# Kernel optimization log

Measured on AMD Instinct MI355X. Metric: run time of the kernel, lower is better.

## Reference

```python
import jax, jax.numpy as jnp
import numpy as np

N_NODES = 100000
N_EDGES = 400000
IN_F, HID, OUT_F = 128, 1024, 64


def gcn_conv(x, src, dst, ew, W, b, n):
    # PyG GCNConv: add self-loops (weight 1), symmetric normalization,
    # out[dst] += norm * (x @ W)[src], then bias.
    loop = jnp.arange(n)
    s = jnp.concatenate([src, loop])
    d = jnp.concatenate([dst, loop])
    w = jnp.concatenate([ew, jnp.ones((n,), dtype=ew.dtype)])
    deg = jax.ops.segment_sum(w, d, num_segments=n)
    dinv = jnp.where(deg > 0, jax.lax.rsqrt(deg), 0.0)
    norm = dinv[s] * w * dinv[d]                      # [E+N]
    h = x @ W                                         # [N, out]
    out = jax.ops.segment_sum(h[s] * norm[:, None], d, num_segments=n)
    return out + b


def setup_inputs() -> dict:
    key = jax.random.key(0)
    k = jax.random.split(key, 8)
    x = jax.random.normal(k[0], (N_NODES, IN_F), dtype=jnp.float32)
    edge_index = jax.random.randint(k[1], (2, N_EDGES), 0, N_NODES, dtype=jnp.int64)
    edge_weight = jax.random.uniform(k[2], (N_EDGES,), dtype=jnp.float32)
    # Glorot-ish init for params
    W1 = jax.random.normal(k[3], (IN_F, HID), dtype=jnp.float32) * (1.0 / np.sqrt(IN_F))
    b1 = jnp.zeros((HID,), dtype=jnp.float32)
    W2 = jax.random.normal(k[4], (HID, OUT_F), dtype=jnp.float32) * (1.0 / np.sqrt(HID))
    b2 = jnp.zeros((OUT_F,), dtype=jnp.float32)
    return {"x": x, "edge_index": edge_index, "edge_weight": edge_weight,
            "W1": W1, "b1": b1, "W2": W2, "b2": b2}


def reference(x, edge_index, edge_weight, W1, b1, W2, b2):
    src, dst = edge_index[0], edge_index[1]
    h = gcn_conv(x, src, dst, edge_weight, W1, b1, N_NODES)
    h = jax.nn.relu(h)
    # F.dropout with training=False is identity (eval mode)
    out = gcn_conv(h, src, dst, edge_weight, W2, b2, N_NODES)
    return out
```

## Files before the change

kernel.cpp:

```cpp
#include <hip/hip_runtime.h>
#include <hip/hip_bf16.h>

#define N_NODES 100000
#define N_EDGES 400000
#define IN_F    128
#define HID     1024
#define OUT_F   64
#define BUCKET_CAP 24

typedef __attribute__((ext_vector_type(8))) short short8;
typedef __attribute__((ext_vector_type(4))) float floatx4;

__device__ inline unsigned short f2bf(float f) {
    unsigned int u = __float_as_uint(f);
    unsigned int r = u + 0x7FFF + ((u >> 16) & 1);
    return (unsigned short)(r >> 16);
}

__device__ inline float bf2f(unsigned int lo16) {
    return __uint_as_float(lo16 << 16);
}

__device__ __forceinline__ void gload_lds16(const void* g, void* l) {
    __builtin_amdgcn_global_load_lds(
        (const __attribute__((address_space(1))) void*)g,
        (__attribute__((address_space(3))) void*)l, 16, 0, 0);
}


__global__ void init_kernel(float* __restrict__ deg, int* __restrict__ cnt, int n) {
    int i = blockIdx.x * blockDim.x + threadIdx.x;
    if (i < n) { deg[i] = 1.0f; cnt[i] = 0; }
}

__global__ void deg_accum_kernel(const int* __restrict__ dst, const float* __restrict__ w,
                                 float* __restrict__ deg, int E) {
    int e = blockIdx.x * blockDim.x + threadIdx.x;
    if (e < E) atomicAdd(&deg[dst[e]], w[e]);
}

__global__ void rsqrt_inplace_kernel(float* __restrict__ deg, int n) {
    int i = blockIdx.x * blockDim.x + threadIdx.x;
    if (i < n) deg[i] = rsqrtf(deg[i]);
}

__global__ void fill_pairs_kernel(const int* __restrict__ src, const int* __restrict__ dst,
                                  const float* __restrict__ w, const float* __restrict__ dinv,
                                  int* __restrict__ cnt, int2* __restrict__ pairs, int E) {
    int e = blockIdx.x * blockDim.x + threadIdx.x;
    if (e < E) {
        int s = src[e];
        int d = dst[e];
        float nv = dinv[s] * w[e] * dinv[d];
        int slot = atomicAdd(&cnt[d], 1);
        if (slot < BUCKET_CAP)
            pairs[(long)d * BUCKET_CAP + slot] = make_int2(s, __float_as_int(nv));
    }
}


__global__ void convert_xb_kernel(const float* __restrict__ in, unsigned short* __restrict__ out, long n8) {
    long i = (long)blockIdx.x * blockDim.x + threadIdx.x;
    if (i < n8) {
        float4 a = ((const float4*)in)[i * 2];
        float4 b = ((const float4*)in)[i * 2 + 1];
        unsigned int q0 = (unsigned int)f2bf(a.x) | ((unsigned int)f2bf(a.y) << 16);
        unsigned int q1 = (unsigned int)f2bf(a.z) | ((unsigned int)f2bf(a.w) << 16);
        unsigned int q2 = (unsigned int)f2bf(b.x) | ((unsigned int)f2bf(b.y) << 16);
        unsigned int q3 = (unsigned int)f2bf(b.z) | ((unsigned int)f2bf(b.w) << 16);
        ((uint4*)out)[i] = make_uint4(q0, q1, q2, q3);
    }
}


__global__ __launch_bounds__(256) void gather128_kernel(
    const int2* __restrict__ pairs, const int* __restrict__ cnt,
    const float* __restrict__ dinv, const unsigned short* __restrict__ xb,
    unsigned short* __restrict__ xab)
{
    int node = blockIdx.x * 4 + (threadIdx.x >> 6);
    int l = threadIdx.x & 63;
    float di = dinv[node];
    float s = di * di;
    unsigned int uv = ((const unsigned int*)(xb + (long)node * IN_F))[l];
    float2 acc;
    acc.x = bf2f(uv & 0xffffu) * s;
    acc.y = bf2f(uv >> 16) * s;
    int c = cnt[node]; c = c < BUCKET_CAP ? c : BUCKET_CAP;
    const int2* p = pairs + (long)node * BUCKET_CAP;
    int j = 0;
    for (; j + 4 <= c; j += 4) {
        int2 p0 = p[j], p1 = p[j + 1], p2 = p[j + 2], p3 = p[j + 3];
        unsigned int u0 = ((const unsigned int*)(xb + (long)p0.x * IN_F))[l];
        unsigned int u1 = ((const unsigned int*)(xb + (long)p1.x * IN_F))[l];
        unsigned int u2 = ((const unsigned int*)(xb + (long)p2.x * IN_F))[l];
        unsigned int u3 = ((const unsigned int*)(xb + (long)p3.x * IN_F))[l];
        float n0 = __int_as_float(p0.y), n1 = __int_as_float(p1.y);
        float n2 = __int_as_float(p2.y), n3 = __int_as_float(p3.y);
        acc.x += n0 * bf2f(u0 & 0xffffu) + n1 * bf2f(u1 & 0xffffu)
               + n2 * bf2f(u2 & 0xffffu) + n3 * bf2f(u3 & 0xffffu);
        acc.y += n0 * bf2f(u0 >> 16) + n1 * bf2f(u1 >> 16)
               + n2 * bf2f(u2 >> 16) + n3 * bf2f(u3 >> 16);
    }
    for (; j < c; j++) {
        int2 pp = p[j];
        float nv = __int_as_float(pp.y);
        unsigned int u = ((const unsigned int*)(xb + (long)pp.x * IN_F))[l];
        acc.x += nv * bf2f(u & 0xffffu);
        acc.y += nv * bf2f(u >> 16);
    }
    unsigned int pk = (unsigned int)f2bf(acc.x) | ((unsigned int)f2bf(acc.y) << 16);
    ((unsigned int*)(xab + (long)node * IN_F))[l] = pk;
}

__global__ __launch_bounds__(256) void gather64_kernel(
    const int2* __restrict__ pairs, const int* __restrict__ cnt,
    const float* __restrict__ dinv, const unsigned short* __restrict__ tb,
    const float* __restrict__ bias, float* __restrict__ out)
{
    int node = blockIdx.x * 8 + (threadIdx.x >> 5);
    int l = threadIdx.x & 31;
    float di = dinv[node];
    float s = di * di;
    unsigned int tv = ((const unsigned int*)(tb + (long)node * OUT_F))[l];
    float2 bb = ((const float2*)bias)[l];
    float2 acc;
    acc.x = bf2f(tv & 0xffffu) * s + bb.x;
    acc.y = bf2f(tv >> 16) * s + bb.y;
    int c = cnt[node]; c = c < BUCKET_CAP ? c : BUCKET_CAP;
    const int2* p = pairs + (long)node * BUCKET_CAP;
    int j = 0;
    for (; j + 4 <= c; j += 4) {
        int2 p0 = p[j], p1 = p[j + 1], p2 = p[j + 2], p3 = p[j + 3];
        unsigned int u0 = ((const unsigned int*)(tb + (long)p0.x * OUT_F))[l];
        unsigned int u1 = ((const unsigned int*)(tb + (long)p1.x * OUT_F))[l];
        unsigned int u2 = ((const unsigned int*)(tb + (long)p2.x * OUT_F))[l];
        unsigned int u3 = ((const unsigned int*)(tb + (long)p3.x * OUT_F))[l];
        float n0 = __int_as_float(p0.y), n1 = __int_as_float(p1.y);
        float n2 = __int_as_float(p2.y), n3 = __int_as_float(p3.y);
        acc.x += n0 * bf2f(u0 & 0xffffu) + n1 * bf2f(u1 & 0xffffu)
               + n2 * bf2f(u2 & 0xffffu) + n3 * bf2f(u3 & 0xffffu);
        acc.y += n0 * bf2f(u0 >> 16) + n1 * bf2f(u1 >> 16)
               + n2 * bf2f(u2 >> 16) + n3 * bf2f(u3 >> 16);
    }
    for (; j < c; j++) {
        int2 pp = p[j];
        float nv = __int_as_float(pp.y);
        unsigned int u = ((const unsigned int*)(tb + (long)pp.x * OUT_F))[l];
        acc.x += nv * bf2f(u & 0xffffu);
        acc.y += nv * bf2f(u >> 16);
    }
    ((float2*)(out + (long)node * OUT_F))[l] = acc;
}


__global__ void convert_wstream_kernel(const float* __restrict__ W1, const float* __restrict__ W2,
                                       unsigned short* __restrict__ S) {
    int r = blockIdx.x * blockDim.x + threadIdx.x;
    int c = blockIdx.y;
    int f = r >> 9;
    int l = (r >> 3) & 63;
    int j = r & 7;
    float v;
    if (f < 16) {
        int nt = f >> 2, kt = f & 3;
        int hid = c * 64 + nt * 16 + (l & 15);
        int k   = kt * 32 + (l >> 4) * 8 + j;
        v = W1[(long)k * HID + hid];
    } else {
        int f2 = f - 16;
        int kb = f2 >> 2, nt = f2 & 3;
        int kh = c * 64 + kb * 32 + (l >> 4) * 8 + j;
        int oc = nt * 16 + (l & 15);
        v = W2[(long)kh * OUT_F + oc];
    }
    S[(long)c * 12288 + r] = f2bf(v);
}


__global__ __launch_bounds__(512, 4) void fused_mlp_mfma_kernel(
    const unsigned short* __restrict__ Xb, const unsigned short* __restrict__ Wstream,
    const float* __restrict__ b1, unsigned short* __restrict__ Tb, int M)
{
    __shared__ unsigned short Wbuf[12288];
    __shared__ unsigned short Hs[8][2048];

    const int tid = threadIdx.x;
    const int w   = tid >> 6;
    const int l   = tid & 63;
    const int lr  = l & 15;
    const int lq  = l >> 4;
    const int swz = (lr & 7) << 4;
    const long row0 = (long)blockIdx.x * 256 + w * 32;

    short8 bx[2][4];
    #pragma unroll
    for (int rt = 0; rt < 2; rt++) {
        long row = row0 + rt * 16 + lr;
        if (row < M) {
            const unsigned short* p = Xb + row * IN_F + lq * 8;
            #pragma unroll
            for (int kt = 0; kt < 4; kt++)
                bx[rt][kt] = *(const short8*)(p + kt * 32);
        } else {
            #pragma unroll
            for (int kt = 0; kt < 4; kt++)
                #pragma unroll
                for (int j = 0; j < 8; j++) bx[rt][kt][j] = 0;
        }
    }

    {
        const unsigned short* g = Wstream + (long)(w * 3) * 512 + l * 8;
        unsigned short* d = &Wbuf[(w * 3) * 512];
        #pragma unroll
        for (int s = 0; s < 3; s++)
            gload_lds16(g + s * 512, d + s * 512);
    }

    floatx4 tacc[2][4];
    #pragma unroll
    for (int rt = 0; rt < 2; rt++)
        #pragma unroll
        for (int nt = 0; nt < 4; nt++)
            tacc[rt][nt] = (floatx4)0.0f;

    for (int c = 0; c < 16; c++) {
        __syncthreads();

        const unsigned short* Wb = &Wbuf[0];
        char* slab = (char*)&Hs[w][0];

        floatx4 hacc[2][4];
        #pragma unroll
        for (int rt = 0; rt < 2; rt++)
            #pragma unroll
            for (int nt = 0; nt < 4; nt++)
                hacc[rt][nt] = (floatx4)0.0f;

        #pragma unroll
        for (int nt = 0; nt < 4; nt++) {
            short8 w1f[4];
            #pragma unroll
            for (int kt = 0; kt < 4; kt++)
                w1f[kt] = *(const short8*)(Wb + (nt * 4 + kt) * 512 + l * 8);
            #pragma unroll
            for (int kt = 0; kt < 4; kt++) {
                hacc[0][nt] = __builtin_amdgcn_mfma_f32_16x16x32_bf16(w1f[kt], bx[0][kt], hacc[0][nt], 0, 0, 0);
                hacc[1][nt] = __builtin_amdgcn_mfma_f32_16x16x32_bf16(w1f[kt], bx[1][kt], hacc[1][nt], 0, 0, 0);
            }
        }

        #pragma unroll
        for (int nt = 0; nt < 4; nt++) {
            floatx4 bb = *(const floatx4*)(b1 + c * 64 + nt * 16 + lq * 4);
            #pragma unroll
            for (int rt = 0; rt < 2; rt++) {
                float h0 = fmaxf(hacc[rt][nt][0] + bb[0], 0.0f);
                float h1 = fmaxf(hacc[rt][nt][1] + bb[1], 0.0f);
                float h2 = fmaxf(hacc[rt][nt][2] + bb[2], 0.0f);
                float h3 = fmaxf(hacc[rt][nt][3] + bb[3], 0.0f);
                unsigned int p0 = (unsigned int)f2bf(h0) | ((unsigned int)f2bf(h1) << 16);
                unsigned int p1 = (unsigned int)f2bf(h2) | ((unsigned int)f2bf(h3) << 16);
                int off = (rt * 16 + lr) * 128 + (((nt * 32) + lq * 8) ^ swz);
                *(uint2*)(slab + off) = make_uint2(p0, p1);
            }
        }

        short8 hf[2][2];
        #pragma unroll
        for (int rt = 0; rt < 2; rt++)
            #pragma unroll
            for (int kb = 0; kb < 2; kb++) {
                int off = (rt * 16 + lr) * 128 + ((kb * 64 + lq * 16) ^ swz);
                hf[rt][kb] = *(const short8*)(slab + off);
            }

        #pragma unroll
        for (int kb = 0; kb < 2; kb++) {
            #pragma unroll
            for (int nt = 0; nt < 4; nt++) {
                short8 w2f = *(const short8*)(Wb + (16 + kb * 4 + nt) * 512 + l * 8);
                tacc[0][nt] = __builtin_amdgcn_mfma_f32_16x16x32_bf16(w2f, hf[0][kb], tacc[0][nt], 0, 0, 0);
                tacc[1][nt] = __builtin_amdgcn_mfma_f32_16x16x32_bf16(w2f, hf[1][kb], tacc[1][nt], 0, 0, 0);
            }
        }

        if (c < 15) {
            __syncthreads();
            const unsigned short* g = Wstream + (long)(c + 1) * 12288 + (long)(w * 3) * 512 + l * 8;
            unsigned short* d = &Wbuf[(w * 3) * 512];
            #pragma unroll
            for (int s = 0; s < 3; s++)
                gload_lds16(g + s * 512, d + s * 512);
        }
    }

    #pragma unroll
    for (int rt = 0; rt < 2; rt++) {
        long row = row0 + rt * 16 + lr;
        if (row < M) {
            #pragma unroll
            for (int nt = 0; nt < 4; nt++) {
                unsigned int q0 = (unsigned int)f2bf(tacc[rt][nt][0]) | ((unsigned int)f2bf(tacc[rt][nt][1]) << 16);
                unsigned int q1 = (unsigned int)f2bf(tacc[rt][nt][2]) | ((unsigned int)f2bf(tacc[rt][nt][3]) << 16);
                *(uint2*)(Tb + row * OUT_F + nt * 16 + lq * 4) = make_uint2(q0, q1);
            }
        }
    }
}


extern "C" void kernel_launch(void* const* d_in, const int* in_sizes, int n_in,
                              void* d_out, int out_size, void* d_ws, size_t ws_size,
                              hipStream_t stream) {
    const float* x   = (const float*)d_in[0];
    const int*   src = (const int*)d_in[1];
    const int*   dst = ((const int*)d_in[1]) + N_EDGES;
    const float* ew  = (const float*)d_in[2];
    const float* W1  = (const float*)d_in[3];
    const float* b1  = (const float*)d_in[4];
    const float* W2  = (const float*)d_in[5];
    const float* b2  = (const float*)d_in[6];
    float* out = (float*)d_out;

    float* ws     = (float*)d_ws;
    float* dinv   = ws;
    int*   cnt    = (int*)(ws + 100096);
    int2*  pairs  = (int2*)(ws + 200192);
    unsigned short* xb  = (unsigned short*)(ws + 5000192);
    unsigned short* xab = (unsigned short*)(ws + 11400192);
    unsigned short* tb  = (unsigned short*)(ws + 17800192);
    unsigned short* wstream = (unsigned short*)(ws + 21000192);

    const int B = 256;

    init_kernel<<<(N_NODES + B - 1) / B, B, 0, stream>>>(dinv, cnt, N_NODES);
    deg_accum_kernel<<<(N_EDGES + B - 1) / B, B, 0, stream>>>(dst, ew, dinv, N_EDGES);
    convert_xb_kernel<<<(int)(((long)N_NODES * IN_F / 8 + B - 1) / B), B, 0, stream>>>(
        x, xb, (long)N_NODES * IN_F / 8);
    convert_wstream_kernel<<<dim3(48, 16), B, 0, stream>>>(W1, W2, wstream);
    rsqrt_inplace_kernel<<<(N_NODES + B - 1) / B, B, 0, stream>>>(dinv, N_NODES);
    fill_pairs_kernel<<<(N_EDGES + B - 1) / B, B, 0, stream>>>(src, dst, ew, dinv, cnt, pairs, N_EDGES);

    gather128_kernel<<<N_NODES / 4, 256, 0, stream>>>(pairs, cnt, dinv, xb, xab);

    fused_mlp_mfma_kernel<<<(N_NODES + 255) / 256, 512, 0, stream>>>(
        xab, wstream, b1, tb, N_NODES);

    gather64_kernel<<<N_NODES / 8, 256, 0, stream>>>(pairs, cnt, dinv, tb, b2, out);
}
```

Before: 184.6 us.

## Double-buffer weight stream and feed hidden activations to MFMA from registers

The fused MLP kernel now double-buffers the LDS weight chunk so the next chunk's global-to-LDS load is issued before computing the current one, removing one barrier per iteration. It also drops the per-wave LDS scratch for the hidden tile: the W2 stream is re-permuted in the conversion kernel so the first MFMA's output register layout maps directly onto the second MFMA's B operand, which avoids the LDS write/read round trip. In exchange the kernel uses about twice the weight LDS, which may change occupancy, and it relies on a more intricate K-index permutation of W2.

```diff
diff --git a/kernel.cpp b/kernel.cpp
--- a/kernel.cpp
+++ b/kernel.cpp
@@ -169,9 +169,9 @@
         v = W1[(long)k * HID + hid];
     } else {
         int f2 = f - 16;
-        int kb = f2 >> 2, nt = f2 & 3;
-        int kh = c * 64 + kb * 32 + (l >> 4) * 8 + j;
-        int oc = nt * 16 + (l & 15);
+        int kb = f2 >> 2, nt2 = f2 & 3;
+        int kh = c * 64 + kb * 32 + (j >> 2) * 16 + (l >> 4) * 4 + (j & 3);
+        int oc = nt2 * 16 + (l & 15);
         v = W2[(long)kh * OUT_F + oc];
     }
     S[(long)c * 12288 + r] = f2bf(v);
@@ -182,15 +182,13 @@
     const unsigned short* __restrict__ Xb, const unsigned short* __restrict__ Wstream,
     const float* __restrict__ b1, unsigned short* __restrict__ Tb, int M)
 {
-    __shared__ unsigned short Wbuf[12288];
-    __shared__ unsigned short Hs[8][2048];
+    __shared__ unsigned short Wbuf[2][12288];
 
     const int tid = threadIdx.x;
     const int w   = tid >> 6;
     const int l   = tid & 63;
     const int lr  = l & 15;
     const int lq  = l >> 4;
-    const int swz = (lr & 7) << 4;
     const long row0 = (long)blockIdx.x * 256 + w * 32;
 
     short8 bx[2][4];
@@ -212,11 +210,12 @@
 
     {
         const unsigned short* g = Wstream + (long)(w * 3) * 512 + l * 8;
-        unsigned short* d = &Wbuf[(w * 3) * 512];
+        unsigned short* d = &Wbuf[0][(w * 3) * 512];
         #pragma unroll
         for (int s = 0; s < 3; s++)
             gload_lds16(g + s * 512, d + s * 512);
     }
+    __syncthreads();
 
     floatx4 tacc[2][4];
     #pragma unroll
@@ -226,74 +225,60 @@
             tacc[rt][nt] = (floatx4)0.0f;
 
     for (int c = 0; c < 16; c++) {
-        __syncthreads();
-
-        const unsigned short* Wb = &Wbuf[0];
-        char* slab = (char*)&Hs[w][0];
-
-        floatx4 hacc[2][4];
-        #pragma unroll
-        for (int rt = 0; rt < 2; rt++)
-            #pragma unroll
-            for (int nt = 0; nt < 4; nt++)
-                hacc[rt][nt] = (floatx4)0.0f;
-
-        #pragma unroll
-        for (int nt = 0; nt < 4; nt++) {
-            short8 w1f[4];
-            #pragma unroll
-            for (int kt = 0; kt < 4; kt++)
-                w1f[kt] = *(const short8*)(Wb + (nt * 4 + kt) * 512 + l * 8);
-            #pragma unroll
-            for (int kt = 0; kt < 4; kt++) {
-                hacc[0][nt] = __builtin_amdgcn_mfma_f32_16x16x32_bf16(w1f[kt], bx[0][kt], hacc[0][nt], 0, 0, 0);
-                hacc[1][nt] = __builtin_amdgcn_mfma_f32_16x16x32_bf16(w1f[kt], bx[1][kt], hacc[1][nt], 0, 0, 0);
-            }
-        }
-
-        #pragma unroll
-        for (int nt = 0; nt < 4; nt++) {
-            floatx4 bb = *(const floatx4*)(b1 + c * 64 + nt * 16 + lq * 4);
-            #pragma unroll
-            for (int rt = 0; rt < 2; rt++) {
-                float h0 = fmaxf(hacc[rt][nt][0] + bb[0], 0.0f);
-                float h1 = fmaxf(hacc[rt][nt][1] + bb[1], 0.0f);
-                float h2 = fmaxf(hacc[rt][nt][2] + bb[2], 0.0f);
-                float h3 = fmaxf(hacc[rt][nt][3] + bb[3], 0.0f);
-                unsigned int p0 = (unsigned int)f2bf(h0) | ((unsigned int)f2bf(h1) << 16);
-                unsigned int p1 = (unsigned int)f2bf(h2) | ((unsigned int)f2bf(h3) << 16);
-                int off = (rt * 16 + lr) * 128 + (((nt * 32) + lq * 8) ^ swz);
-                *(uint2*)(slab + off) = make_uint2(p0, p1);
-            }
-        }
-
-        short8 hf[2][2];
-        #pragma unroll
-        for (int rt = 0; rt < 2; rt++)
-            #pragma unroll
-            for (int kb = 0; kb < 2; kb++) {
-                int off = (rt * 16 + lr) * 128 + ((kb * 64 + lq * 16) ^ swz);
-                hf[rt][kb] = *(const short8*)(slab + off);
-            }
-
-        #pragma unroll
-        for (int kb = 0; kb < 2; kb++) {
-            #pragma unroll
-            for (int nt = 0; nt < 4; nt++) {
-                short8 w2f = *(const short8*)(Wb + (16 + kb * 4 + nt) * 512 + l * 8);
-                tacc[0][nt] = __builtin_amdgcn_mfma_f32_16x16x32_bf16(w2f, hf[0][kb], tacc[0][nt], 0, 0, 0);
-                tacc[1][nt] = __builtin_amdgcn_mfma_f32_16x16x32_bf16(w2f, hf[1][kb], tacc[1][nt], 0, 0, 0);
-            }
-        }
+        const unsigned short* Wb = &Wbuf[c & 1][0];
 
         if (c < 15) {
-            __syncthreads();
             const unsigned short* g = Wstream + (long)(c + 1) * 12288 + (long)(w * 3) * 512 + l * 8;
-            unsigned short* d = &Wbuf[(w * 3) * 512];
+            unsigned short* d = &Wbuf[(c + 1) & 1][(w * 3) * 512];
             #pragma unroll
             for (int s = 0; s < 3; s++)
                 gload_lds16(g + s * 512, d + s * 512);
         }
+
+        #pragma unroll
+        for (int h = 0; h < 2; h++) {
+            floatx4 hacc[2][2];
+            #pragma unroll
+            for (int rt = 0; rt < 2; rt++)
+                #pragma unroll
+                for (int n = 0; n < 2; n++)
+                    hacc[rt][n] = (floatx4)0.0f;
+
+            #pragma unroll
+            for (int n = 0; n < 2; n++) {
+                const int nt = h * 2 + n;
+                short8 w1f[4];
+                #pragma unroll
+                for (int kt = 0; kt < 4; kt++)
+                    w1f[kt] = *(const short8*)(Wb + (nt * 4 + kt) * 512 + l * 8);
+                #pragma unroll
+                for (int kt = 0; kt < 4; kt++) {
+                    hacc[0][n] = __builtin_amdgcn_mfma_f32_16x16x32_bf16(w1f[kt], bx[0][kt], hacc[0][n], 0, 0, 0);
+                    hacc[1][n] = __builtin_amdgcn_mfma_f32_16x16x32_bf16(w1f[kt], bx[1][kt], hacc[1][n], 0, 0, 0);
+                }
+            }
+
+            floatx4 bb0 = *(const floatx4*)(b1 + c * 64 + (h * 2 + 0) * 16 + lq * 4);
+            floatx4 bb1 = *(const floatx4*)(b1 + c * 64 + (h * 2 + 1) * 16 + lq * 4);
+            short8 hf[2];
+            #pragma unroll
+            for (int rt = 0; rt < 2; rt++) {
+                #pragma unroll
+                for (int r = 0; r < 4; r++) {
+                    hf[rt][r]     = (short)f2bf(fmaxf(hacc[rt][0][r] + bb0[r], 0.0f));
+                    hf[rt][r + 4] = (short)f2bf(fmaxf(hacc[rt][1][r] + bb1[r], 0.0f));
+                }
+            }
+
+            #pragma unroll
+            for (int nt2 = 0; nt2 < 4; nt2++) {
+                short8 w2f = *(const short8*)(Wb + (16 + h * 4 + nt2) * 512 + l * 8);
+                tacc[0][nt2] = __builtin_amdgcn_mfma_f32_16x16x32_bf16(w2f, hf[0], tacc[0][nt2], 0, 0, 0);
+                tacc[1][nt2] = __builtin_amdgcn_mfma_f32_16x16x32_bf16(w2f, hf[1], tacc[1][nt2], 0, 0, 0);
+            }
+        }
+
+        if (c < 15) __syncthreads();
     }
 
     #pragma unroll
```

Result: faster. 176.6 us (-4.3%).
